# Performance work log

Hardware: AMD Instinct MI355X
Metric: run time of the kernel (lower is better)

The kernel has to match this reference:

```python
import jax, jax.numpy as jnp
import numpy as np

N_NODES = 100000
N_EDGES = 1600000
N_FEAT = 128
HIDDEN = 128
N_GRAPHS = 64
N_CLASSES = 10
BN_EPS = 1e-5


def setup_inputs() -> dict:
    key = jax.random.key(0)
    ks = jax.random.split(key, 24)
    glorot = lambda k, o, i: jax.random.normal(k, (o, i), jnp.float32) * (1.0 / np.sqrt(i))
    inp = {
        'x': jax.random.normal(ks[0], (N_NODES, N_FEAT), jnp.float32),
        'edge_index': jax.random.randint(ks[1], (2, N_EDGES), 0, N_NODES, jnp.int64),
        'batch': jnp.sort(jax.random.randint(ks[2], (N_NODES,), 0, N_GRAPHS, jnp.int64)),
        # GCNConv(128 -> 128)
        'gcn_w': glorot(ks[3], HIDDEN, N_FEAT),
        'gcn_b': jnp.zeros((HIDDEN,), jnp.float32),
        # SAGEConv layers 1, 2: lin_l (aggregated, with bias) + lin_r (root, no bias)
        'sage1_wl': glorot(ks[4], HIDDEN, HIDDEN),
        'sage1_bl': jnp.zeros((HIDDEN,), jnp.float32),
        'sage1_wr': glorot(ks[5], HIDDEN, HIDDEN),
        'sage2_wl': glorot(ks[6], HIDDEN, HIDDEN),
        'sage2_bl': jnp.zeros((HIDDEN,), jnp.float32),
        'sage2_wr': glorot(ks[7], HIDDEN, HIDDEN),
        # ClassifierBase: 128 -> 200 -> 100 -> 50 -> 10
        'clf_w0': glorot(ks[8], 200, HIDDEN), 'clf_b0': jnp.zeros((200,), jnp.float32),
        'clf_w1': glorot(ks[9], 100, 200), 'clf_b1': jnp.zeros((100,), jnp.float32),
        'clf_w2': glorot(ks[10], 50, 100), 'clf_b2': jnp.zeros((50,), jnp.float32),
        'clf_w3': glorot(ks[11], N_CLASSES, 50), 'clf_b3': jnp.zeros((N_CLASSES,), jnp.float32),
        # BatchNorm1d (eval mode, running_mean=0, running_var=1)
        'bn0_g': jnp.ones((200,), jnp.float32), 'bn0_b': jnp.zeros((200,), jnp.float32),
        'bn1_g': jnp.ones((100,), jnp.float32), 'bn1_b': jnp.zeros((100,), jnp.float32),
        'bn2_g': jnp.ones((50,), jnp.float32), 'bn2_b': jnp.zeros((50,), jnp.float32),
    }
    return inp


def _gcn_conv(x, src, dst, W, b):
    # PyG GCNConv: add self loops, symmetric deg^{-1/2} normalization
    xw = x @ W.T                                                  # [N, H]
    ones = jnp.ones(src.shape[0], xw.dtype)
    deg = jax.ops.segment_sum(ones, dst, num_segments=N_NODES) + 1.0  # self loops
    dinv = jax.lax.rsqrt(deg)
    norm = dinv[src] * dinv[dst]                                  # [E]
    out = jax.ops.segment_sum(xw[src] * norm[:, None], dst, num_segments=N_NODES)
    out = out + xw * (dinv * dinv)[:, None]                       # self-loop term deg^{-1}
    return out + b


def _sage_conv(x, src, dst, Wl, bl, Wr):
    # PyG SAGEConv (mean aggr): lin_l(mean_{j->i} x_j) + lin_r(x_i)
    ones = jnp.ones(src.shape[0], x.dtype)
    cnt = jax.ops.segment_sum(ones, dst, num_segments=N_NODES)
    agg = jax.ops.segment_sum(x[src], dst, num_segments=N_NODES)
    agg = agg / jnp.maximum(cnt, 1.0)[:, None]
    return agg @ Wl.T + bl + x @ Wr.T


def _bn_eval(h, g, b):
    # eval-mode BatchNorm1d with running_mean=0, running_var=1
    return h * (g / np.sqrt(1.0 + BN_EPS)) + b


def reference(x, edge_index, batch, gcn_w, gcn_b,
              sage1_wl, sage1_bl, sage1_wr, sage2_wl, sage2_bl, sage2_wr,
              clf_w0, clf_b0, clf_w1, clf_b1, clf_w2, clf_b2, clf_w3, clf_b3,
              bn0_g, bn0_b, bn1_g, bn1_b, bn2_g, bn2_b):
    src, dst = edge_index[0], edge_index[1]
    h = _gcn_conv(x, src, dst, gcn_w, gcn_b)          # act_func is None -> no activation
    h = _sage_conv(h, src, dst, sage1_wl, sage1_bl, sage1_wr)
    h = _sage_conv(h, src, dst, sage2_wl, sage2_bl, sage2_wr)
    # global mean pool over graphs
    gcnt = jax.ops.segment_sum(jnp.ones(h.shape[0], h.dtype), batch, num_segments=N_GRAPHS)
    g = jax.ops.segment_sum(h, batch, num_segments=N_GRAPHS) / jnp.maximum(gcnt, 1.0)[:, None]
    # ClassifierBase (eval: dropout inactive), tanh activation
    g = jnp.tanh(_bn_eval(g @ clf_w0.T + clf_b0, bn0_g, bn0_b))
    g = jnp.tanh(_bn_eval(g @ clf_w1.T + clf_b1, bn1_g, bn1_b))
    g = jnp.tanh(_bn_eval(g @ clf_w2.T + clf_b2, bn2_g, bn2_b))
    logits = g @ clf_w3.T + clf_b3
    return jax.nn.softmax(logits, axis=1)             # [B, n_classes]
```

## Files before the change

### kernel.cpp

```cpp
#include <hip/hip_runtime.h>

#define N_NODES 100000
#define N_EDGES 1600000
#define NGRAPH 64
#define NBIN 391
#define EPB 2560
#define NBLK 625
#define CAPB 6144
#define CAPP 7168
#define PSPLIT 8
#define SETUPBLK 1600

typedef short s8v __attribute__((ext_vector_type(8)));
typedef float f4v __attribute__((ext_vector_type(4)));
typedef float f2v __attribute__((ext_vector_type(2)));

__device__ __forceinline__ float bflo(unsigned u) { return __uint_as_float(u << 16); }
__device__ __forceinline__ float bfhi(unsigned u) { return __uint_as_float(u & 0xffff0000u); }
__device__ __forceinline__ unsigned short f2bf(float f) {
    unsigned u = __float_as_uint(f);
    u += 0x7fffu + ((u >> 16) & 1u);
    return (unsigned short)(u >> 16);
}
__device__ __forceinline__ float bf2f(unsigned short h) { return __uint_as_float(((unsigned)h) << 16); }
__device__ __forceinline__ unsigned pk(float lo, float hi) {
    return (unsigned)f2bf(lo) | ((unsigned)f2bf(hi) << 16);
}
__device__ __forceinline__ float ldv(const void* p, int i, int f32) {
    return f32 ? ((const float*)p)[i] : bf2f(((const unsigned short*)p)[i]);
}
__device__ __forceinline__ f2v up2(unsigned u) {
    f2v t; t.x = bflo(u); t.y = bfhi(u); return t;
}

__global__ __launch_bounds__(256) void k_setup(const unsigned short* __restrict__ x,
                                               const int* __restrict__ ei,
                                               const int* __restrict__ batch,
                                               int* __restrict__ flags,
                                               int* __restrict__ binCur,
                                               int* __restrict__ gstart,
                                               float* __restrict__ pbuf,
                                               float* __restrict__ wbuf,
                                               unsigned* __restrict__ xcvt,
                                               const void* w0, const void* w1,
                                               const void* w2, const void* w3,
                                               const void* b0, const void* bn0g, const void* bn0b,
                                               const void* b1, const void* bn1g, const void* bn1b,
                                               const void* b2, const void* bn2g, const void* bn2b,
                                               const void* b3) {
    __shared__ int cnt[3];
    int tid = threadIdx.x, bid = blockIdx.x;
    if (tid < 3) cnt[tid] = 0;
    __syncthreads();
    unsigned short h = x[tid * 37];
    int e = (h >> 7) & 0xFF;
    if (e >= 100 && e <= 150) atomicAdd(&cnt[0], 1);
    if (bid == 0) {
        if (ei[2 * (tid * 5000) + 1] == 0) atomicAdd(&cnt[1], 1);
        if (batch[2 * (tid * 193) + 1] == 0) atomicAdd(&cnt[2], 1);
    }
    __syncthreads();
    int f = (cnt[0] == 256) ? 0 : 1;
    int i = bid * 256 + tid;
    if (i < 25600) wbuf[i] = ldv(w0, i, f);
    else if (i < 45600) wbuf[i] = ldv(w1, i - 25600, f);
    else if (i < 50600) wbuf[i] = ldv(w2, i - 45600, f);
    else if (i < 51100) wbuf[i] = ldv(w3, i - 50600, f);
    if (f) {
        for (int id = bid * 256 + tid; id < N_NODES * 64; id += SETUPBLK * 256) {
            float2 u = ((const float2*)x)[id];
            xcvt[id] = pk(u.x, u.y);
        }
    }
    if (bid != 0) return;
    int b64 = (cnt[2] == 256) ? 1 : 0;
    if (tid == 0) {
        flags[0] = f;
        flags[1] = (cnt[1] == 256) ? 1 : 0;
        flags[2] = b64;
    }
    for (int k = tid; k < NBIN; k += 256) binCur[k] = 0;
    if (tid <= NGRAPH) {
        int g = tid, lo = 0, hi = N_NODES;
        while (lo < hi) {
            int mid = (lo + hi) >> 1;
            int v = b64 ? batch[2 * mid] : batch[mid];
            if (v < g) lo = mid + 1;
            else hi = mid;
        }
        gstart[g] = lo;
    }
    const float invs = rsqrtf(1.0f + 1e-5f);
    if (tid < 200) {
        float a = ldv(bn0g, tid, f) * invs;
        pbuf[tid] = a;
        pbuf[200 + tid] = ldv(b0, tid, f) * a + ldv(bn0b, tid, f);
    }
    if (tid < 100) {
        float a = ldv(bn1g, tid, f) * invs;
        pbuf[400 + tid] = a;
        pbuf[500 + tid] = ldv(b1, tid, f) * a + ldv(bn1b, tid, f);
    }
    if (tid < 50) {
        float a = ldv(bn2g, tid, f) * invs;
        pbuf[600 + tid] = a;
        pbuf[650 + tid] = ldv(b2, tid, f) * a + ldv(bn2b, tid, f);
    }
    if (tid < 10) pbuf[700 + tid] = ldv(b3, tid, f);
}

__global__ __launch_bounds__(256) void k_binfill(const int* __restrict__ ei,
                                                 int* __restrict__ binCur,
                                                 unsigned* __restrict__ staging,
                                                 const int* __restrict__ flags) {
    __shared__ int cnt[NBIN];
    __shared__ int basg[NBIN];
    __shared__ int dbuf[EPB];
    int tid = threadIdx.x;
    int i64 = flags[1];
    int base = blockIdx.x * EPB;
    for (int i = tid; i < NBIN; i += 256) cnt[i] = 0;
    __syncthreads();
    #pragma unroll
    for (int k = 0; k < EPB / 512; ++k) {
        int e = base + k * 512 + tid * 2;
        int d0, d1;
        if (i64) {
            uint4 vd = *(const uint4*)(ei + 2 * (size_t)(N_EDGES + e));
            d0 = (int)vd.x; d1 = (int)vd.z;
        } else {
            int2 vd = *(const int2*)(ei + (size_t)N_EDGES + e);
            d0 = vd.x; d1 = vd.y;
        }
        int l = k * 512 + tid * 2;
        dbuf[l] = d0; dbuf[l + 1] = d1;
        if ((unsigned)d0 < N_NODES) atomicAdd(&cnt[d0 >> 8], 1);
        if ((unsigned)d1 < N_NODES) atomicAdd(&cnt[d1 >> 8], 1);
    }
    __syncthreads();
    for (int i = tid; i < NBIN; i += 256) {
        int c = cnt[i];
        basg[i] = i * CAPB + (c ? atomicAdd(&binCur[i], c) : 0);
        cnt[i] = 0;
    }
    __syncthreads();
    #pragma unroll
    for (int k = 0; k < EPB / 512; ++k) {
        int e = base + k * 512 + tid * 2;
        int s0, s1;
        if (i64) {
            uint4 vs = *(const uint4*)(ei + 2 * (size_t)e);
            s0 = (int)vs.x; s1 = (int)vs.z;
        } else {
            int2 vs = *(const int2*)(ei + (size_t)e);
            s0 = vs.x; s1 = vs.y;
        }
        int l = k * 512 + tid * 2;
        #pragma unroll
        for (int hh = 0; hh < 2; ++hh) {
            int d = dbuf[l + hh];
            int s = hh ? s1 : s0;
            if ((unsigned)d < N_NODES) {
                s = min(max(s, 0), N_NODES - 1);
                int b = d >> 8;
                int p = atomicAdd(&cnt[b], 1);
                int pos = basg[b] + p;
                if (pos < (b + 1) * CAPB)
                    staging[pos] = ((unsigned)(d & 255) << 20) | (unsigned)s;
            }
        }
    }
}

__global__ __launch_bounds__(256) void k_csr(const unsigned* __restrict__ staging,
                                             const int* __restrict__ binCur,
                                             int2* __restrict__ rse,
                                             float* __restrict__ dinv,
                                             int* __restrict__ colidx,
                                             unsigned* __restrict__ padA,
                                             unsigned* __restrict__ padB) {
    __shared__ int deg[256];
    __shared__ int s[256];
    __shared__ int cur[256];
    __shared__ int colbuf[CAPP];
    int b = blockIdx.x, tid = threadIdx.x;
    int n0 = b << 8;
    int nend = min(256, N_NODES - n0);
    int runStart = b * CAPB;
    int outStart = b * CAPP;
    int runLen = min(binCur[b], CAPB);
    deg[tid] = 0;
    for (int i = tid; i < CAPP; i += 256) colbuf[i] = N_NODES;
    __syncthreads();
    for (int i = tid; i < runLen; i += 256)
        atomicAdd(&deg[staging[runStart + i] >> 20], 1);
    __syncthreads();
    int myDeg = deg[tid];
    int pdeg = (myDeg + 15) & ~15;
    s[tid] = pdeg;
    __syncthreads();
    for (int off = 1; off < 256; off <<= 1) {
        int x2 = (tid >= off) ? s[tid - off] : 0;
        __syncthreads();
        s[tid] += x2;
        __syncthreads();
    }
    int incl = s[tid];
    int lrs = incl - pdeg;
    if (tid < nend) {
        rse[n0 + tid] = make_int2(outStart + lrs, outStart + lrs + myDeg);
        dinv[n0 + tid] = rsqrtf((float)myDeg + 1.0f);
    }
    cur[tid] = lrs;
    __syncthreads();
    for (int i = tid; i < runLen; i += 256) {
        unsigned e = staging[runStart + i];
        int p = atomicAdd(&cur[e >> 20], 1);
        if (p < CAPP) colbuf[p] = (int)(e & 0xFFFFF);
    }
    __syncthreads();
    int ptot = min(s[255], CAPP);
    for (int i = tid; i < ptot; i += 256) colidx[outStart + i] = colbuf[i];
    if (b == 0) {
        if (tid < 64) {
            padA[(size_t)N_NODES * 64 + tid] = 0u;
            padB[(size_t)N_NODES * 64 + tid] = 0u;
        }
        if (tid == 0) dinv[N_NODES] = 0.f;
    }
}

template <int MODE>
__global__ __launch_bounds__(256) void k_agg(const uint4* __restrict__ xsA,
                                             const uint4* __restrict__ xsB,
                                             const int2* __restrict__ rse,
                                             const float* __restrict__ dinv,
                                             unsigned* __restrict__ out,
                                             const int* __restrict__ col,
                                             const int* __restrict__ flags) {
    int lane = threadIdx.x & 63;
    int node = blockIdx.x * 4 + (threadIdx.x >> 6);
    int glane = lane & 15, grp = lane >> 4;
    const uint4* xs = (MODE == 0) ? (flags[0] ? xsB : xsA) : xsA;
    int2 rr = rse[node];
    int rs = rr.x, deg = rr.y - rr.x;
    int pend = rs + ((deg + 15) & ~15);
    f2v a0 = {0.f, 0.f}, a1 = {0.f, 0.f}, a2 = {0.f, 0.f}, a3 = {0.f, 0.f};
    uint4 selfu = make_uint4(0u, 0u, 0u, 0u);
    float di = 0.f;
    if (MODE == 0) {
        selfu = xs[(unsigned)node * 16u + glane];
        di = dinv[node];
    }

    for (int base = rs; base < pend; base += 16) {
        int4 c = *(const int4*)(col + base + grp * 4);
        float dv0, dv1, dv2, dv3;
        if (MODE == 0) {
            dv0 = dinv[c.x]; dv1 = dinv[c.y]; dv2 = dinv[c.z]; dv3 = dinv[c.w];
            c.x = min(c.x, N_NODES - 1); c.y = min(c.y, N_NODES - 1);
            c.z = min(c.z, N_NODES - 1); c.w = min(c.w, N_NODES - 1);
        }
        uint4 u0 = xs[(unsigned)c.x * 16u + glane];
        uint4 u1 = xs[(unsigned)c.y * 16u + glane];
        uint4 u2 = xs[(unsigned)c.z * 16u + glane];
        uint4 u3 = xs[(unsigned)c.w * 16u + glane];
        if (MODE == 0) {
            a0 += dv0 * up2(u0.x); a1 += dv0 * up2(u0.y); a2 += dv0 * up2(u0.z); a3 += dv0 * up2(u0.w);
            a0 += dv1 * up2(u1.x); a1 += dv1 * up2(u1.y); a2 += dv1 * up2(u1.z); a3 += dv1 * up2(u1.w);
            a0 += dv2 * up2(u2.x); a1 += dv2 * up2(u2.y); a2 += dv2 * up2(u2.z); a3 += dv2 * up2(u2.w);
            a0 += dv3 * up2(u3.x); a1 += dv3 * up2(u3.y); a2 += dv3 * up2(u3.z); a3 += dv3 * up2(u3.w);
        } else {
            a0 += up2(u0.x); a1 += up2(u0.y); a2 += up2(u0.z); a3 += up2(u0.w);
            a0 += up2(u1.x); a1 += up2(u1.y); a2 += up2(u1.z); a3 += up2(u1.w);
            a0 += up2(u2.x); a1 += up2(u2.y); a2 += up2(u2.z); a3 += up2(u2.w);
            a0 += up2(u3.x); a1 += up2(u3.y); a2 += up2(u3.z); a3 += up2(u3.w);
        }
    }
    float r[8] = {a0.x, a0.y, a1.x, a1.y, a2.x, a2.y, a3.x, a3.y};
    #pragma unroll
    for (int i = 0; i < 8; ++i) {
        float v = r[i];
        v += __shfl_xor(v, 16, 64);
        v += __shfl_xor(v, 32, 64);
        r[i] = v;
    }
    if (MODE == 0) {
        float d2 = di * di;
        r[0] = di * r[0] + d2 * bflo(selfu.x); r[1] = di * r[1] + d2 * bfhi(selfu.x);
        r[2] = di * r[2] + d2 * bflo(selfu.y); r[3] = di * r[3] + d2 * bfhi(selfu.y);
        r[4] = di * r[4] + d2 * bflo(selfu.z); r[5] = di * r[5] + d2 * bfhi(selfu.z);
        r[6] = di * r[6] + d2 * bflo(selfu.w); r[7] = di * r[7] + d2 * bfhi(selfu.w);
    } else {
        float s = 1.0f / fmaxf((float)deg, 1.0f);
        #pragma unroll
        for (int i = 0; i < 8; ++i) r[i] *= s;
    }
    if (grp == 0) {
        uint4 o;
        o.x = pk(r[0], r[1]); o.y = pk(r[2], r[3]);
        o.z = pk(r[4], r[5]); o.w = pk(r[6], r[7]);
        *(uint4*)(out + (size_t)node * 64 + glane * 4) = o;
    }
}

template <int DUAL>
__global__ __launch_bounds__(512) void k_gemm(const unsigned short* __restrict__ A0,
                                              const void* __restrict__ W0,
                                              const unsigned short* __restrict__ A1,
                                              const void* __restrict__ W1,
                                              const void* __restrict__ bias,
                                              unsigned short* __restrict__ out,
                                              const int* __restrict__ flags) {
    __shared__ __align__(16) unsigned short Ws[128][136];
    int f32 = flags[0];
    int tid = threadIdx.x;
    int lane = tid & 63;
    int wave = tid >> 6;
    int rowbase = blockIdx.x * 128;
    int lr = lane & 15, q = lane >> 4;
    int m0 = wave * 16;
    int arow = rowbase + m0 + lr;
    if (arow > N_NODES) arow = N_NODES;

    f4v acc[8];
    #pragma unroll
    for (int t = 0; t < 8; ++t) acc[t] = (f4v){0.f, 0.f, 0.f, 0.f};

    #pragma unroll
    for (int p = 0; p < (DUAL ? 2 : 1); ++p) {
        const unsigned short* Ap = p ? A1 : A0;
        const void* Wp = p ? W1 : W0;
        if (p) __syncthreads();
        if (!f32) {
            const unsigned short* Wf = (const unsigned short*)Wp;
            #pragma unroll
            for (int it = 0; it < 4; ++it) {
                int chunk = tid + it * 512;
                int r = chunk >> 4, c8 = (chunk & 15) * 8;
                *(uint4*)&Ws[r][c8] = *(const uint4*)(Wf + r * 128 + c8);
            }
        } else {
            const float* Wf = (const float*)Wp;
            #pragma unroll
            for (int it = 0; it < 8; ++it) {
                int chunk = tid + it * 512;
                int r = chunk >> 5, c4 = (chunk & 31) * 4;
                float4 v = *(const float4*)(Wf + r * 128 + c4);
                *(uint2*)&Ws[r][c4] = make_uint2(pk(v.x, v.y), pk(v.z, v.w));
            }
        }
        const unsigned short* Arp = Ap + (size_t)arow * 128;
        s8v a[4];
        #pragma unroll
        for (int k = 0; k < 4; ++k) a[k] = *(const s8v*)(Arp + k * 32 + q * 8);
        __syncthreads();
        #pragma unroll
        for (int k = 0; k < 4; ++k) {
            #pragma unroll
            for (int t = 0; t < 8; ++t) {
                s8v b = *(const s8v*)&Ws[t * 16 + lr][k * 32 + q * 8];
                acc[t] = __builtin_amdgcn_mfma_f32_16x16x32_bf16(a[k], b, acc[t], 0, 0, 0);
            }
        }
    }
    #pragma unroll
    for (int t = 0; t < 8; ++t) {
        int o = t * 16 + lr;
        float bv = ldv(bias, o, f32);
        #pragma unroll
        for (int j = 0; j < 4; ++j) {
            int m = rowbase + m0 + q * 4 + j;
            if (m < N_NODES) out[(size_t)m * 128 + o] = f2bf(acc[t][j] + bv);
        }
    }
}

__global__ __launch_bounds__(256) void k_pool2(const unsigned* __restrict__ h,
                                               const int* __restrict__ gstart,
                                               float* __restrict__ ppool) {
    __shared__ float part[4][128];
    int g = blockIdx.x / PSPLIT, sl = blockIdx.x % PSPLIT;
    int wave = threadIdx.x >> 6, lane = threadIdx.x & 63;
    int s0 = gstart[g], s1 = gstart[g + 1];
    int n = s1 - s0;
    int chunk = (n + PSPLIT - 1) / PSPLIT;
    int r0 = s0 + sl * chunk;
    int r1 = min(r0 + chunk, s1);
    float a0 = 0.f, a1 = 0.f;
    for (int r = r0 + wave; r < r1; r += 4) {
        unsigned u = h[(size_t)r * 64 + lane];
        a0 += bflo(u);
        a1 += bfhi(u);
    }
    part[wave][2 * lane] = a0;
    part[wave][2 * lane + 1] = a1;
    __syncthreads();
    int t = threadIdx.x;
    if (t < 128) {
        float s = part[0][t] + part[1][t] + part[2][t] + part[3][t];
        ppool[(size_t)blockIdx.x * 128 + t] = s;
    }
}

__global__ __launch_bounds__(256) void k_clf(const float* __restrict__ ppool,
                                             const int* __restrict__ gstart,
                                             const float* __restrict__ wbuf,
                                             const float* __restrict__ pbuf,
                                             void* outv, const int* __restrict__ flags) {
    __shared__ float gin[128];
    __shared__ float ha[200];
    __shared__ float hb[100];
    int b = blockIdx.x, t = threadIdx.x;
    if (t < 128) {
        float s = 0.f;
        #pragma unroll
        for (int k = 0; k < PSPLIT; ++k) s += ppool[(size_t)(b * PSPLIT + k) * 128 + t];
        int cnt = gstart[b + 1] - gstart[b];
        gin[t] = s / fmaxf((float)cnt, 1.0f);
    }
    __syncthreads();
    if (t < 200) {
        const float4* wr = (const float4*)(wbuf + t * 128);
        float s = 0.f;
        #pragma unroll
        for (int k = 0; k < 32; ++k) {
            float4 v = wr[k];
            s += v.x * gin[4 * k] + v.y * gin[4 * k + 1] + v.z * gin[4 * k + 2] + v.w * gin[4 * k + 3];
        }
        ha[t] = tanhf(s * pbuf[t] + pbuf[200 + t]);
    }
    __syncthreads();
    if (t < 100) {
        const float4* wr = (const float4*)(wbuf + 25600 + t * 200);
        float s = 0.f;
        #pragma unroll
        for (int k = 0; k < 50; ++k) {
            float4 v = wr[k];
            s += v.x * ha[4 * k] + v.y * ha[4 * k + 1] + v.z * ha[4 * k + 2] + v.w * ha[4 * k + 3];
        }
        hb[t] = tanhf(s * pbuf[400 + t] + pbuf[500 + t]);
    }
    __syncthreads();
    if (t < 50) {
        const float4* wr = (const float4*)(wbuf + 45600 + t * 100);
        float s = 0.f;
        #pragma unroll
        for (int k = 0; k < 25; ++k) {
            float4 v = wr[k];
            s += v.x * hb[4 * k] + v.y * hb[4 * k + 1] + v.z * hb[4 * k + 2] + v.w * hb[4 * k + 3];
        }
        gin[t] = tanhf(s * pbuf[600 + t] + pbuf[650 + t]);
    }
    __syncthreads();
    if (t == 0) {
        int f = flags[0];
        float lg[10];
        float mx = -1e30f;
        #pragma unroll
        for (int c = 0; c < 10; ++c) {
            const float* wr = wbuf + 50600 + c * 50;
            float s = 0.f;
            for (int k = 0; k < 50; ++k) s += wr[k] * gin[k];
            s += pbuf[700 + c];
            lg[c] = s;
            mx = fmaxf(mx, s);
        }
        float sum = 0.f;
        #pragma unroll
        for (int c = 0; c < 10; ++c) {
            lg[c] = __expf(lg[c] - mx);
            sum += lg[c];
        }
        float inv = 1.0f / sum;
        #pragma unroll
        for (int c = 0; c < 10; ++c) {
            float v = lg[c] * inv;
            if (f) ((float*)outv)[b * 10 + c] = v;
            else ((unsigned short*)outv)[b * 10 + c] = f2bf(v);
        }
    }
}

extern "C" void kernel_launch(void* const* d_in, const int* in_sizes, int n_in,
                              void* d_out, int out_size, void* d_ws, size_t ws_size,
                              hipStream_t stream) {
    const unsigned short* x16 = (const unsigned short*)d_in[0];
    const int* ei = (const int*)d_in[1];
    const int* batch = (const int*)d_in[2];

    char* ws = (char*)d_ws;
    size_t off = 0;
    auto alloc = [&](size_t bytes) {
        size_t r = off;
        off = (off + bytes + 255) & ~(size_t)255;
        return r;
    };
    int* flags = (int*)(ws + alloc(256));
    int2* rse = (int2*)(ws + alloc((size_t)N_NODES * 8));
    int* colidx = (int*)(ws + alloc((size_t)NBIN * CAPP * 4 + (size_t)CAPP * 4));
    float* dinv = (float*)(ws + alloc((size_t)(N_NODES + 1) * 4));
    int* binCur = (int*)(ws + alloc(NBIN * 4));
    int* gstart = (int*)(ws + alloc((NGRAPH + 1) * 4));
    float* pbuf = (float*)(ws + alloc(710 * 4));
    float* ppool = (float*)(ws + alloc((size_t)NGRAPH * PSPLIT * 128 * 4));
    float* wbuf = (float*)(ws + alloc(51100 * 4));
    unsigned short* bufA = (unsigned short*)(ws + alloc((size_t)(N_NODES + 1) * 128 * 2));
    unsigned short* bufB = (unsigned short*)(ws + alloc((size_t)(N_NODES + 1) * 128 * 2));
    unsigned* staging = (unsigned*)bufA;

    k_setup<<<SETUPBLK, 256, 0, stream>>>(x16, ei, batch, flags, binCur, gstart, pbuf, wbuf,
                                          (unsigned*)bufB,
                                          d_in[11], d_in[13], d_in[15], d_in[17],
                                          d_in[12], d_in[19], d_in[20],
                                          d_in[14], d_in[21], d_in[22],
                                          d_in[16], d_in[23], d_in[24], d_in[18]);

    k_binfill<<<NBLK, 256, 0, stream>>>(ei, binCur, staging, flags);
    k_csr<<<NBIN, 256, 0, stream>>>(staging, binCur, rse, dinv, colidx,
                                    (unsigned*)bufA, (unsigned*)bufB);

    k_agg<0><<<N_NODES / 4, 256, 0, stream>>>((const uint4*)x16, (const uint4*)bufB,
                                              rse, dinv, (unsigned*)bufA, colidx, flags);
    k_gemm<0><<<(N_NODES + 127) / 128, 512, 0, stream>>>(bufA, d_in[3], nullptr, nullptr,
                                                         d_in[4], bufA, flags);
    k_agg<1><<<N_NODES / 4, 256, 0, stream>>>((const uint4*)bufA, (const uint4*)bufA,
                                              rse, dinv, (unsigned*)bufB, colidx, flags);
    k_gemm<1><<<(N_NODES + 127) / 128, 512, 0, stream>>>(bufB, d_in[5], bufA, d_in[7],
                                                         d_in[6], bufB, flags);
    k_agg<1><<<N_NODES / 4, 256, 0, stream>>>((const uint4*)bufB, (const uint4*)bufB,
                                              rse, dinv, (unsigned*)bufA, colidx, flags);
    k_gemm<1><<<(N_NODES + 127) / 128, 512, 0, stream>>>(bufA, d_in[8], bufB, d_in[10],
                                                         d_in[9], bufA, flags);
    k_pool2<<<NGRAPH * PSPLIT, 256, 0, stream>>>((const unsigned*)bufA, gstart, ppool);
    k_clf<<<NGRAPH, 256, 0, stream>>>(ppool, gstart, wbuf, pbuf, d_out, flags);
}
```

Before: 465.6 us.

## Fuse mean-pool into final SAGE GEMM epilogue and use wave-shuffle scan in CSR

The last GEMM no longer writes the 100k x 128 bf16 activations. Its epilogue instead accumulates per-graph sums in shared memory with atomics and flushes them to a global per-graph sum buffer, which removes the separate pooling kernel and one full activation read. The CSR build swaps the block-wide shared-memory prefix scan for a wavefront shuffle scan, and only the padding slots of colbuf are filled rather than the whole buffer. The cost is heavy shared-memory atomic contention in the GEMM epilogue, and float atomics make the summation order nondeterministic.

```diff
diff --git a/kernel.cpp b/kernel.cpp
--- a/kernel.cpp
+++ b/kernel.cpp
@@ -8,7 +8,6 @@
 #define NBLK 625
 #define CAPB 6144
 #define CAPP 7168
-#define PSPLIT 8
 #define SETUPBLK 1600
 
 typedef short s8v __attribute__((ext_vector_type(8)));
@@ -42,6 +41,7 @@
                                                float* __restrict__ pbuf,
                                                float* __restrict__ wbuf,
                                                unsigned* __restrict__ xcvt,
+                                               float* __restrict__ pgsum,
                                                const void* w0, const void* w1,
                                                const void* w2, const void* w3,
                                                const void* b0, const void* bn0g, const void* bn0b,
@@ -80,6 +80,7 @@
         flags[2] = b64;
     }
     for (int k = tid; k < NBIN; k += 256) binCur[k] = 0;
+    for (int k = tid; k < NGRAPH * 128; k += 256) pgsum[k] = 0.f;
     if (tid <= NGRAPH) {
         int g = tid, lo = 0, hi = N_NODES;
         while (lo < hi) {
@@ -180,38 +181,42 @@
                                              unsigned* __restrict__ padA,
                                              unsigned* __restrict__ padB) {
     __shared__ int deg[256];
-    __shared__ int s[256];
     __shared__ int cur[256];
+    __shared__ int wsum[4];
     __shared__ int colbuf[CAPP];
     int b = blockIdx.x, tid = threadIdx.x;
+    int lane = tid & 63, wv = tid >> 6;
     int n0 = b << 8;
     int nend = min(256, N_NODES - n0);
     int runStart = b * CAPB;
     int outStart = b * CAPP;
     int runLen = min(binCur[b], CAPB);
     deg[tid] = 0;
-    for (int i = tid; i < CAPP; i += 256) colbuf[i] = N_NODES;
     __syncthreads();
     for (int i = tid; i < runLen; i += 256)
         atomicAdd(&deg[staging[runStart + i] >> 20], 1);
     __syncthreads();
     int myDeg = deg[tid];
     int pdeg = (myDeg + 15) & ~15;
-    s[tid] = pdeg;
-    __syncthreads();
-    for (int off = 1; off < 256; off <<= 1) {
-        int x2 = (tid >= off) ? s[tid - off] : 0;
-        __syncthreads();
-        s[tid] += x2;
-        __syncthreads();
-    }
-    int incl = s[tid];
+    int v = pdeg;
+    #pragma unroll
+    for (int off = 1; off < 64; off <<= 1) {
+        int n = __shfl_up(v, off, 64);
+        if (lane >= off) v += n;
+    }
+    if (lane == 63) wsum[wv] = v;
+    __syncthreads();
+    int prefix = 0;
+    #pragma unroll
+    for (int w = 0; w < 4; ++w) prefix += (w < wv) ? wsum[w] : 0;
+    int incl = v + prefix;
     int lrs = incl - pdeg;
     if (tid < nend) {
         rse[n0 + tid] = make_int2(outStart + lrs, outStart + lrs + myDeg);
         dinv[n0 + tid] = rsqrtf((float)myDeg + 1.0f);
     }
     cur[tid] = lrs;
+    for (int p = lrs + myDeg; p < lrs + pdeg; ++p) colbuf[p] = N_NODES;
     __syncthreads();
     for (int i = tid; i < runLen; i += 256) {
         unsigned e = staging[runStart + i];
@@ -219,7 +224,7 @@
         if (p < CAPP) colbuf[p] = (int)(e & 0xFFFFF);
     }
     __syncthreads();
-    int ptot = min(s[255], CAPP);
+    int ptot = min(wsum[0] + wsum[1] + wsum[2] + wsum[3], CAPP);
     for (int i = tid; i < ptot; i += 256) colidx[outStart + i] = colbuf[i];
     if (b == 0) {
         if (tid < 64) {
@@ -304,14 +309,16 @@
     }
 }
 
-template <int DUAL>
+template <int DUAL, int POOL>
 __global__ __launch_bounds__(512) void k_gemm(const unsigned short* __restrict__ A0,
                                               const void* __restrict__ W0,
                                               const unsigned short* __restrict__ A1,
                                               const void* __restrict__ W1,
                                               const void* __restrict__ bias,
                                               unsigned short* __restrict__ out,
-                                              const int* __restrict__ flags) {
+                                              const int* __restrict__ flags,
+                                              const int* __restrict__ gstart,
+                                              float* __restrict__ pgsum) {
     __shared__ __align__(16) unsigned short Ws[128][136];
     int f32 = flags[0];
     int tid = threadIdx.x;
@@ -364,46 +371,55 @@
             }
         }
     }
-    #pragma unroll
-    for (int t = 0; t < 8; ++t) {
-        int o = t * 16 + lr;
-        float bv = ldv(bias, o, f32);
+    if (!POOL) {
+        #pragma unroll
+        for (int t = 0; t < 8; ++t) {
+            int o = t * 16 + lr;
+            float bv = ldv(bias, o, f32);
+            #pragma unroll
+            for (int j = 0; j < 4; ++j) {
+                int m = rowbase + m0 + q * 4 + j;
+                if (m < N_NODES) out[(size_t)m * 128 + o] = f2bf(acc[t][j] + bv);
+            }
+        }
+    } else {
+        float* segf = (float*)&Ws[0][0];
+        __syncthreads();
+        segf[tid] = 0.f;
+        __syncthreads();
+        int gLo;
+        {
+            int lo = 0, hi = NGRAPH - 1;
+            while (lo < hi) { int mid = (lo + hi + 1) >> 1; if (gstart[mid] <= rowbase) lo = mid; else hi = mid - 1; }
+            gLo = lo;
+        }
+        int g = gLo;
         #pragma unroll
         for (int j = 0; j < 4; ++j) {
             int m = rowbase + m0 + q * 4 + j;
-            if (m < N_NODES) out[(size_t)m * 128 + o] = f2bf(acc[t][j] + bv);
-        }
-    }
-}
-
-__global__ __launch_bounds__(256) void k_pool2(const unsigned* __restrict__ h,
-                                               const int* __restrict__ gstart,
-                                               float* __restrict__ ppool) {
-    __shared__ float part[4][128];
-    int g = blockIdx.x / PSPLIT, sl = blockIdx.x % PSPLIT;
-    int wave = threadIdx.x >> 6, lane = threadIdx.x & 63;
-    int s0 = gstart[g], s1 = gstart[g + 1];
-    int n = s1 - s0;
-    int chunk = (n + PSPLIT - 1) / PSPLIT;
-    int r0 = s0 + sl * chunk;
-    int r1 = min(r0 + chunk, s1);
-    float a0 = 0.f, a1 = 0.f;
-    for (int r = r0 + wave; r < r1; r += 4) {
-        unsigned u = h[(size_t)r * 64 + lane];
-        a0 += bflo(u);
-        a1 += bfhi(u);
-    }
-    part[wave][2 * lane] = a0;
-    part[wave][2 * lane + 1] = a1;
-    __syncthreads();
-    int t = threadIdx.x;
-    if (t < 128) {
-        float s = part[0][t] + part[1][t] + part[2][t] + part[3][t];
-        ppool[(size_t)blockIdx.x * 128 + t] = s;
-    }
-}
-
-__global__ __launch_bounds__(256) void k_clf(const float* __restrict__ ppool,
+            if (m < N_NODES) {
+                while (gstart[g + 1] <= m) ++g;
+                int s = g - gLo;
+                #pragma unroll
+                for (int t = 0; t < 8; ++t) {
+                    int o = t * 16 + lr;
+                    float val = acc[t][j] + ldv(bias, o, f32);
+                    if (s < 4) atomicAdd(&segf[s * 128 + o], val);
+                    else atomicAdd(&pgsum[g * 128 + o], val);
+                }
+            }
+        }
+        __syncthreads();
+        int s = tid >> 7, o = tid & 127;
+        int g2 = gLo + s;
+        if (g2 < NGRAPH) {
+            float vv = segf[tid];
+            if (vv != 0.f) atomicAdd(&pgsum[g2 * 128 + o], vv);
+        }
+    }
+}
+
+__global__ __launch_bounds__(256) void k_clf(const float* __restrict__ pgsum,
                                              const int* __restrict__ gstart,
                                              const float* __restrict__ wbuf,
                                              const float* __restrict__ pbuf,
@@ -413,11 +429,8 @@
     __shared__ float hb[100];
     int b = blockIdx.x, t = threadIdx.x;
     if (t < 128) {
-        float s = 0.f;
-        #pragma unroll
-        for (int k = 0; k < PSPLIT; ++k) s += ppool[(size_t)(b * PSPLIT + k) * 128 + t];
         int cnt = gstart[b + 1] - gstart[b];
-        gin[t] = s / fmaxf((float)cnt, 1.0f);
+        gin[t] = pgsum[b * 128 + t] / fmaxf((float)cnt, 1.0f);
     }
     __syncthreads();
     if (t < 200) {
@@ -503,14 +516,14 @@
     int* binCur = (int*)(ws + alloc(NBIN * 4));
     int* gstart = (int*)(ws + alloc((NGRAPH + 1) * 4));
     float* pbuf = (float*)(ws + alloc(710 * 4));
-    float* ppool = (float*)(ws + alloc((size_t)NGRAPH * PSPLIT * 128 * 4));
+    float* pgsum = (float*)(ws + alloc((size_t)NGRAPH * 128 * 4));
     float* wbuf = (float*)(ws + alloc(51100 * 4));
     unsigned short* bufA = (unsigned short*)(ws + alloc((size_t)(N_NODES + 1) * 128 * 2));
     unsigned short* bufB = (unsigned short*)(ws + alloc((size_t)(N_NODES + 1) * 128 * 2));
     unsigned* staging = (unsigned*)bufA;
 
     k_setup<<<SETUPBLK, 256, 0, stream>>>(x16, ei, batch, flags, binCur, gstart, pbuf, wbuf,
-                                          (unsigned*)bufB,
+                                          (unsigned*)bufB, pgsum,
                                           d_in[11], d_in[13], d_in[15], d_in[17],
                                           d_in[12], d_in[19], d_in[20],
                                           d_in[14], d_in[21], d_in[22],
@@ -522,16 +535,15 @@
 
     k_agg<0><<<N_NODES / 4, 256, 0, stream>>>((const uint4*)x16, (const uint4*)bufB,
                                               rse, dinv, (unsigned*)bufA, colidx, flags);
-    k_gemm<0><<<(N_NODES + 127) / 128, 512, 0, stream>>>(bufA, d_in[3], nullptr, nullptr,
-                                                         d_in[4], bufA, flags);
+    k_gemm<0, 0><<<(N_NODES + 127) / 128, 512, 0, stream>>>(bufA, d_in[3], nullptr, nullptr,
+                                                            d_in[4], bufA, flags, gstart, pgsum);
     k_agg<1><<<N_NODES / 4, 256, 0, stream>>>((const uint4*)bufA, (const uint4*)bufA,
                                               rse, dinv, (unsigned*)bufB, colidx, flags);
-    k_gemm<1><<<(N_NODES + 127) / 128, 512, 0, stream>>>(bufB, d_in[5], bufA, d_in[7],
-                                                         d_in[6], bufB, flags);
+    k_gemm<1, 0><<<(N_NODES + 127) / 128, 512, 0, stream>>>(bufB, d_in[5], bufA, d_in[7],
+                                                            d_in[6], bufB, flags, gstart, pgsum);
     k_agg<1><<<N_NODES / 4, 256, 0, stream>>>((const uint4*)bufB, (const uint4*)bufB,
                                               rse, dinv, (unsigned*)bufA, colidx, flags);
-    k_gemm<1><<<(N_NODES + 127) / 128, 512, 0, stream>>>(bufA, d_in[8], bufB, d_in[10],
-                                                         d_in[9], bufA, flags);
-    k_pool2<<<NGRAPH * PSPLIT, 256, 0, stream>>>((const unsigned*)bufA, gstart, ppool);
-    k_clf<<<NGRAPH, 256, 0, stream>>>(ppool, gstart, wbuf, pbuf, d_out, flags);
-}
+    k_gemm<1, 1><<<(N_NODES + 127) / 128, 512, 0, stream>>>(bufA, d_in[8], bufB, d_in[10],
+                                                            d_in[9], bufA, flags, gstart, pgsum);
+    k_clf<<<NGRAPH, 256, 0, stream>>>(pgsum, gstart, wbuf, pbuf, d_out, flags);
+}
```

New measurement: 524.5 us. 1.13x slower.
